# Kernel tuning notes

Hardware: AMD Instinct MI355X
Metric: run time of the kernel (lower is better)

The kernel has to match this reference:

```python
import jax, jax.numpy as jnp
import numpy as np

N_NODES = 50000
N_EDGES = 1600000
IN_DIM = 128
HID = 64   # per-head hidden/out dim
HEADS = 2
NEG_SLOPE = 0.2


def _gat_layer(x, src, dst, W, attn_l, attn_r, bias):
    # x: [N, Fin]; W: [Fin, H*D]; attn_l/attn_r: [H, D]; bias: [H, D]
    N = x.shape[0]
    H, D = attn_l.shape
    feat = (x @ W).reshape(N, H, D)                      # [N,H,D]
    el = jnp.sum(feat * attn_l, axis=-1)                 # [N,H]
    er = jnp.sum(feat * attn_r, axis=-1)                 # [N,H]
    e = jax.nn.leaky_relu(el[src] + er[dst], NEG_SLOPE)  # [E,H]
    # segment softmax over destination nodes
    m = jax.ops.segment_max(e, dst, num_segments=N)      # [N,H]
    ex = jnp.exp(e - m[dst])                             # [E,H]
    s = jax.ops.segment_sum(ex, dst, num_segments=N)     # [N,H]
    alpha = ex / s[dst]                                  # [E,H]
    msg = feat[src] * alpha[..., None]                   # [E,H,D]
    out = jax.ops.segment_sum(msg, dst, num_segments=N)  # [N,H,D]
    out = out + bias                                     # per-head bias
    # encoder: mean over heads, then ELU
    return jax.nn.elu(out.mean(axis=1))                  # [N,D]


def setup_inputs() -> dict:
    key = jax.random.key(0)
    ks = jax.random.split(key, 12)
    features = jax.random.normal(ks[0], (N_NODES, IN_DIM), dtype=jnp.float32)
    src = jax.random.randint(ks[1], (N_EDGES,), 0, N_NODES, dtype=jnp.int32)
    dst = jax.random.randint(ks[2], (N_EDGES,), 0, N_NODES, dtype=jnp.int32)
    sc1 = 1.0 / np.sqrt(IN_DIM)
    sc2 = 1.0 / np.sqrt(HID)
    W1 = jax.random.normal(ks[3], (IN_DIM, HEADS * HID), dtype=jnp.float32) * sc1
    al1 = jax.random.normal(ks[4], (HEADS, HID), dtype=jnp.float32) * sc2
    ar1 = jax.random.normal(ks[5], (HEADS, HID), dtype=jnp.float32) * sc2
    b1 = jnp.zeros((HEADS, HID), dtype=jnp.float32)
    W2 = jax.random.normal(ks[6], (HID, HEADS * HID), dtype=jnp.float32) * sc2
    al2 = jax.random.normal(ks[7], (HEADS, HID), dtype=jnp.float32) * sc2
    ar2 = jax.random.normal(ks[8], (HEADS, HID), dtype=jnp.float32) * sc2
    b2 = jnp.zeros((HEADS, HID), dtype=jnp.float32)
    return {"features": features, "W1": W1, "al1": al1, "ar1": ar1, "b1": b1,
            "W2": W2, "al2": al2, "ar2": ar2, "b2": b2, "src": src, "dst": dst}


def reference(features, W1, al1, ar1, b1, W2, al2, ar2, b2, src, dst):
    h = _gat_layer(features, src, dst, W1, al1, ar1, b1)  # [N, HID]
    h = _gat_layer(h, src, dst, W2, al2, ar2, b2)         # [N, HID]
    return h
```

## Files before the change

kernel.cpp:

```cpp
#include <hip/hip_runtime.h>
#include <hip/hip_fp16.h>
#include <math.h>

#define N_NODES 50000
#define N_EDGES 1600000
#define SLOTS 96
#define NODES_PER_GRP 6250

typedef int v4i __attribute__((ext_vector_type(4)));


__global__ void zero_kernel(int* p, int n) {
    int i = blockIdx.x * blockDim.x + threadIdx.x;
    if (i < n) p[i] = 0;
}

__global__ __launch_bounds__(256) void fill_part_kernel(
    const int* __restrict__ src, const int* __restrict__ dst,
    int* __restrict__ cursor, int* __restrict__ ssrc, int E) {
    const int g = blockIdx.x & 7;
    const int bg = blockIdx.x >> 3;
    const int nbg = gridDim.x >> 3;
    const int lo = g * NODES_PER_GRP;
    const int hi = lo + NODES_PER_GRP;
    const v4i* d4 = (const v4i*)dst;
    const v4i* s4 = (const v4i*)src;
    const int E4 = E >> 2;

    for (int i = bg * 256 + threadIdx.x; i < E4; i += nbg * 256) {
        v4i d = __builtin_nontemporal_load(d4 + i);
        v4i s = __builtin_nontemporal_load(s4 + i);
        if (d.x >= lo && d.x < hi) {
            int p = atomicAdd(&cursor[d.x], 1);
            if (p < SLOTS) ssrc[d.x * SLOTS + p] = s.x;
        }
        if (d.y >= lo && d.y < hi) {
            int p = atomicAdd(&cursor[d.y], 1);
            if (p < SLOTS) ssrc[d.y * SLOTS + p] = s.y;
        }
        if (d.z >= lo && d.z < hi) {
            int p = atomicAdd(&cursor[d.z], 1);
            if (p < SLOTS) ssrc[d.z * SLOTS + p] = s.z;
        }
        if (d.w >= lo && d.w < hi) {
            int p = atomicAdd(&cursor[d.w], 1);
            if (p < SLOTS) ssrc[d.w * SLOTS + p] = s.w;
        }
    }
}


template <int K>
__global__ __launch_bounds__(256) void gemm_elr_kernel(
    const float* __restrict__ x,
    const float* __restrict__ W,
    const float* __restrict__ al,
    const float* __restrict__ ar,
    __half* __restrict__ feat,
    float* __restrict__ el,
    float* __restrict__ er,
    int N) {
    constexpr int LDX = K + 4;
    __shared__ float xs[32 * LDX];
    const int tid = threadIdx.x;
    const int node0 = blockIdx.x * 32;

    for (int i = tid; i < 32 * K / 4; i += 256) {
        int r = i / (K / 4), c4 = i % (K / 4);
        float4 v = make_float4(0.f, 0.f, 0.f, 0.f);
        if (node0 + r < N) v = *(const float4*)&x[(size_t)(node0 + r) * K + c4 * 4];
        *(float4*)&xs[r * LDX + c4 * 4] = v;
    }
    __syncthreads();

    const int tx = tid & 31;
    const int ty = tid >> 5;
    const int col = tx * 4;

    float acc[4][4];
#pragma unroll
    for (int r = 0; r < 4; ++r)
#pragma unroll
        for (int c = 0; c < 4; ++c) acc[r][c] = 0.f;

    for (int kb = 0; kb < K / 4; ++kb) {
        float4 w0 = *(const float4*)&W[(kb * 4 + 0) * 128 + col];
        float4 w1 = *(const float4*)&W[(kb * 4 + 1) * 128 + col];
        float4 w2 = *(const float4*)&W[(kb * 4 + 2) * 128 + col];
        float4 w3 = *(const float4*)&W[(kb * 4 + 3) * 128 + col];
        float4 xv[4];
#pragma unroll
        for (int r = 0; r < 4; ++r)
            xv[r] = *(const float4*)&xs[(ty * 4 + r) * LDX + kb * 4];
#pragma unroll
        for (int r = 0; r < 4; ++r) {
            acc[r][0] += xv[r].x * w0.x + xv[r].y * w1.x + xv[r].z * w2.x + xv[r].w * w3.x;
            acc[r][1] += xv[r].x * w0.y + xv[r].y * w1.y + xv[r].z * w2.y + xv[r].w * w3.y;
            acc[r][2] += xv[r].x * w0.z + xv[r].y * w1.z + xv[r].z * w2.z + xv[r].w * w3.z;
            acc[r][3] += xv[r].x * w0.w + xv[r].y * w1.w + xv[r].z * w2.w + xv[r].w * w3.w;
        }
    }

    float4 alv = *(const float4*)&al[col];
    float4 arv = *(const float4*)&ar[col];
    float elp[4], erp[4];
#pragma unroll
    for (int r = 0; r < 4; ++r) {
        int n = node0 + ty * 4 + r;
        float4 f = make_float4(acc[r][0], acc[r][1], acc[r][2], acc[r][3]);
        if (n < N) {
            __half2 p0 = __floats2half2_rn(f.x, f.y);
            __half2 p1 = __floats2half2_rn(f.z, f.w);
            union { __half2 h2[2]; uint2 u; } pk;
            pk.h2[0] = p0; pk.h2[1] = p1;
            *(uint2*)&feat[(size_t)n * 128 + col] = pk.u;
        }
        elp[r] = f.x * alv.x + f.y * alv.y + f.z * alv.z + f.w * alv.w;
        erp[r] = f.x * arv.x + f.y * arv.y + f.z * arv.z + f.w * arv.w;
    }
#pragma unroll
    for (int m = 1; m <= 8; m <<= 1) {
#pragma unroll
        for (int r = 0; r < 4; ++r) {
            elp[r] += __shfl_xor(elp[r], m, 64);
            erp[r] += __shfl_xor(erp[r], m, 64);
        }
    }
    int h = tx >> 4;
    if ((tx & 15) == 0) {
#pragma unroll
        for (int r = 0; r < 4; ++r) {
            int n = node0 + ty * 4 + r;
            if (n < N) {
                el[n * 2 + h] = elp[r];
                er[n * 2 + h] = erp[r];
            }
        }
    }
}


__global__ __launch_bounds__(256) void aggregate_kernel(
    const __half* __restrict__ feat,
    const float* __restrict__ el,
    const float* __restrict__ er,
    const int* __restrict__ deg,
    const int* __restrict__ ssrc,
    const float* __restrict__ bias,
    float* __restrict__ hout,
    int N) {
    const int wave = threadIdx.x >> 6;
    const int lane = threadIdx.x & 63;
    const int n = blockIdx.x * 4 + wave;
    if (n >= N) return;

    const int q = lane >> 4;
    const int ql = lane & 15;
    const int h = ql >> 3;
    const float er_h = er[n * 2 + h];
    const int start = n * SLOTS;
    int d = deg[n];
    if (d > SLOTS) d = SLOTS;

    float acc[8];
#pragma unroll
    for (int j = 0; j < 8; ++j) acc[j] = 0.f;
    float ssum = 0.f;

#pragma unroll 2
    for (int base = 0; base < d; base += 4) {
        int idx = base + q;
        bool valid = idx < d;
        int s = ssrc[start + (valid ? idx : 0)];
        float e = el[s * 2 + h] + er_h;
        e = e > 0.f ? e : 0.2f * e;
        float x = valid ? __expf(e) : 0.f;
        float4 raw = *(const float4*)(feat + (size_t)s * 128 + ql * 8);
        const __half2* hp = (const __half2*)&raw;
        float2 f0 = __half22float2(hp[0]);
        float2 f1 = __half22float2(hp[1]);
        float2 f2 = __half22float2(hp[2]);
        float2 f3 = __half22float2(hp[3]);
        ssum += x;
        acc[0] += x * f0.x; acc[1] += x * f0.y;
        acc[2] += x * f1.x; acc[3] += x * f1.y;
        acc[4] += x * f2.x; acc[5] += x * f2.y;
        acc[6] += x * f3.x; acc[7] += x * f3.y;
    }

#pragma unroll
    for (int m = 16; m <= 32; m <<= 1) {
#pragma unroll
        for (int j = 0; j < 8; ++j) acc[j] += __shfl_xor(acc[j], m, 64);
        ssum += __shfl_xor(ssum, m, 64);
    }

    float inv = (d > 0) ? 1.0f / ssum : 0.0f;
    float4 b0 = *(const float4*)&bias[ql * 8];
    float4 b1 = *(const float4*)&bias[ql * 8 + 4];
    float v[8];
    v[0] = acc[0] * inv + b0.x; v[1] = acc[1] * inv + b0.y;
    v[2] = acc[2] * inv + b0.z; v[3] = acc[3] * inv + b0.w;
    v[4] = acc[4] * inv + b1.x; v[5] = acc[5] * inv + b1.y;
    v[6] = acc[6] * inv + b1.z; v[7] = acc[7] * inv + b1.w;

    float o[8];
#pragma unroll
    for (int j = 0; j < 8; ++j) {
        float p = __shfl_xor(v[j], 8, 64);
        float t = 0.5f * (v[j] + p);
        o[j] = t > 0.f ? t : expm1f(t);
    }
    if (lane < 8) {
        float4 w0 = make_float4(o[0], o[1], o[2], o[3]);
        float4 w1 = make_float4(o[4], o[5], o[6], o[7]);
        *(float4*)&hout[(size_t)n * 64 + ql * 8] = w0;
        *(float4*)&hout[(size_t)n * 64 + ql * 8 + 4] = w1;
    }
}


extern "C" void kernel_launch(void* const* d_in, const int* in_sizes, int n_in,
                              void* d_out, int out_size, void* d_ws, size_t ws_size,
                              hipStream_t stream) {
    const float* features = (const float*)d_in[0];
    const float* W1 = (const float*)d_in[1];
    const float* al1 = (const float*)d_in[2];
    const float* ar1 = (const float*)d_in[3];
    const float* b1 = (const float*)d_in[4];
    const float* W2 = (const float*)d_in[5];
    const float* al2 = (const float*)d_in[6];
    const float* ar2 = (const float*)d_in[7];
    const float* b2 = (const float*)d_in[8];
    const int* src = (const int*)d_in[9];
    const int* dst = (const int*)d_in[10];
    float* out = (float*)d_out;

    const int N = N_NODES;
    const int E = N_EDGES;

    char* ws = (char*)d_ws;
    size_t off = 0;
    auto alloc = [&](size_t bytes) {
        void* p = ws + off;
        off = (off + bytes + 255) & ~255ULL;
        return p;
    };
    int* cursor   = (int*)alloc((size_t)N * 4);
    int* ssrc     = (int*)alloc((size_t)N * SLOTS * 4);
    __half* feath = (__half*)alloc((size_t)N * 128 * 2);
    float* el     = (float*)alloc((size_t)N * 2 * 4);
    float* er     = (float*)alloc((size_t)N * 2 * 4);
    float* h1     = (float*)alloc((size_t)N * 64 * 4);

    zero_kernel<<<(N + 255) / 256, 256, 0, stream>>>(cursor, N);
    fill_part_kernel<<<2048, 256, 0, stream>>>(src, dst, cursor, ssrc, E);

    gemm_elr_kernel<128><<<(N + 31) / 32, 256, 0, stream>>>(features, W1, al1, ar1,
                                                            feath, el, er, N);
    aggregate_kernel<<<(N + 3) / 4, 256, 0, stream>>>(feath, el, er, cursor, ssrc,
                                                      b1, h1, N);
    gemm_elr_kernel<64><<<(N + 31) / 32, 256, 0, stream>>>(h1, W2, al2, ar2,
                                                           feath, el, er, N);
    aggregate_kernel<<<(N + 3) / 4, 256, 0, stream>>>(feath, el, er, cursor, ssrc,
                                                      b2, out, N);
}
```

Measured before the change: 412.0 us.

## Register-cache edge chunk and sweep destination sub-ranges in fill kernel

Each block now loads a contiguous chunk of src/dst edge vectors into registers once, then loops over 10 smaller destination-node sub-ranges. Inside each sub-range it issues the atomic cursor updates and slot writes, with a block barrier between sub-ranges. The goal is to tighten the working set of cursor/ssrc lines touched at a time and improve cache locality of scattered atomics. This adds more predicate checks per edge and extra barriers, and removes the nontemporal hints on the edge loads.

After: 547.8 us. +33.0%, slower.

```diff
diff --git a/kernel.cpp b/kernel.cpp
--- a/kernel.cpp
+++ b/kernel.cpp
@@ -6,6 +6,12 @@
 #define N_EDGES 1600000
 #define SLOTS 96
 #define NODES_PER_GRP 6250
+#define SUBS 10
+#define SUBW 625
+#define NBG 256
+#define E4T (N_EDGES / 4)
+#define CHUNK 1563
+#define PT 7
 
 typedef int v4i __attribute__((ext_vector_type(4)));
 
@@ -17,35 +23,53 @@
 
 __global__ __launch_bounds__(256) void fill_part_kernel(
     const int* __restrict__ src, const int* __restrict__ dst,
-    int* __restrict__ cursor, int* __restrict__ ssrc, int E) {
+    int* __restrict__ cursor, int* __restrict__ ssrc) {
     const int g = blockIdx.x & 7;
     const int bg = blockIdx.x >> 3;
-    const int nbg = gridDim.x >> 3;
-    const int lo = g * NODES_PER_GRP;
-    const int hi = lo + NODES_PER_GRP;
+    const int lo0 = g * NODES_PER_GRP;
     const v4i* d4 = (const v4i*)dst;
     const v4i* s4 = (const v4i*)src;
-    const int E4 = E >> 2;
-
-    for (int i = bg * 256 + threadIdx.x; i < E4; i += nbg * 256) {
-        v4i d = __builtin_nontemporal_load(d4 + i);
-        v4i s = __builtin_nontemporal_load(s4 + i);
-        if (d.x >= lo && d.x < hi) {
-            int p = atomicAdd(&cursor[d.x], 1);
-            if (p < SLOTS) ssrc[d.x * SLOTS + p] = s.x;
-        }
-        if (d.y >= lo && d.y < hi) {
-            int p = atomicAdd(&cursor[d.y], 1);
-            if (p < SLOTS) ssrc[d.y * SLOTS + p] = s.y;
-        }
-        if (d.z >= lo && d.z < hi) {
-            int p = atomicAdd(&cursor[d.z], 1);
-            if (p < SLOTS) ssrc[d.z * SLOTS + p] = s.z;
-        }
-        if (d.w >= lo && d.w < hi) {
-            int p = atomicAdd(&cursor[d.w], 1);
-            if (p < SLOTS) ssrc[d.w * SLOTS + p] = s.w;
-        }
+    const int base = bg * CHUNK;
+    const int elim = (base + CHUNK < E4T) ? base + CHUNK : E4T;
+
+    v4i dreg[PT], sreg[PT];
+#pragma unroll
+    for (int j = 0; j < PT; ++j) {
+        int i = base + j * 256 + (int)threadIdx.x;
+        if (i < elim) {
+            dreg[j] = d4[i];
+            sreg[j] = s4[i];
+        } else {
+            dreg[j] = (v4i){-1, -1, -1, -1};
+        }
+    }
+
+#pragma unroll 1
+    for (int sub = 0; sub < SUBS; ++sub) {
+        const int lo = lo0 + sub * SUBW;
+        const int hi = lo + SUBW;
+#pragma unroll
+        for (int j = 0; j < PT; ++j) {
+            v4i d = dreg[j];
+            v4i s = sreg[j];
+            if (d.x >= lo && d.x < hi) {
+                int p = atomicAdd(&cursor[d.x], 1);
+                if (p < SLOTS) ssrc[d.x * SLOTS + p] = s.x;
+            }
+            if (d.y >= lo && d.y < hi) {
+                int p = atomicAdd(&cursor[d.y], 1);
+                if (p < SLOTS) ssrc[d.y * SLOTS + p] = s.y;
+            }
+            if (d.z >= lo && d.z < hi) {
+                int p = atomicAdd(&cursor[d.z], 1);
+                if (p < SLOTS) ssrc[d.z * SLOTS + p] = s.z;
+            }
+            if (d.w >= lo && d.w < hi) {
+                int p = atomicAdd(&cursor[d.w], 1);
+                if (p < SLOTS) ssrc[d.w * SLOTS + p] = s.w;
+            }
+        }
+        __syncthreads();
     }
 }
 
@@ -237,7 +261,6 @@
     float* out = (float*)d_out;
 
     const int N = N_NODES;
-    const int E = N_EDGES;
 
     char* ws = (char*)d_ws;
     size_t off = 0;
@@ -254,7 +277,7 @@
     float* h1     = (float*)alloc((size_t)N * 64 * 4);
 
     zero_kernel<<<(N + 255) / 256, 256, 0, stream>>>(cursor, N);
-    fill_part_kernel<<<2048, 256, 0, stream>>>(src, dst, cursor, ssrc, E);
+    fill_part_kernel<<<NBG * 8, 256, 0, stream>>>(src, dst, cursor, ssrc);
 
     gemm_elr_kernel<128><<<(N + 31) / 32, 256, 0, stream>>>(features, W1, al1, ar1,
                                                             feath, el, er, N);
```

## Partition edge bucketing by hardware XCD with dynamic chunked work stealing

Applied to the files above, without the earlier changes.

The fill kernel used to map node groups to blocks via blockIdx modulo 8. It now reads the hardware XCC ID so each block starts on the node partition owned by its own XCD, which keeps cursor atomics and ssrc writes local to that XCD's L2. Blocks grab 2048-vec4 chunks from per-partition atomic work counters and move on to other partitions once their own is drained. In exchange there are extra __syncthreads and a global atomic per chunk, and the hardware register read depends on the architecture.

Result: slower. 581.6 us (+41.2%).

```diff
diff --git a/kernel.cpp b/kernel.cpp
--- a/kernel.cpp
+++ b/kernel.cpp
@@ -6,6 +6,8 @@
 #define N_EDGES 1600000
 #define SLOTS 96
 #define NODES_PER_GRP 6250
+#define E4T (N_EDGES / 4)
+#define CH4 2048
 
 typedef int v4i __attribute__((ext_vector_type(4)));
 
@@ -15,36 +17,56 @@
     if (i < n) p[i] = 0;
 }
 
-__global__ __launch_bounds__(256) void fill_part_kernel(
+__device__ __forceinline__ int get_xcd() {
+    int x;
+    asm volatile("s_getreg_b32 %0, hwreg(HW_REG_XCC_ID)" : "=s"(x));
+    return x & 7;
+}
+
+__global__ __launch_bounds__(256) void fill_xcd_kernel(
     const int* __restrict__ src, const int* __restrict__ dst,
-    int* __restrict__ cursor, int* __restrict__ ssrc, int E) {
-    const int g = blockIdx.x & 7;
-    const int bg = blockIdx.x >> 3;
-    const int nbg = gridDim.x >> 3;
-    const int lo = g * NODES_PER_GRP;
-    const int hi = lo + NODES_PER_GRP;
+    int* __restrict__ cursor, int* __restrict__ ssrc,
+    int* __restrict__ work) {
+    const int xcd = get_xcd();
     const v4i* d4 = (const v4i*)dst;
     const v4i* s4 = (const v4i*)src;
-    const int E4 = E >> 2;
-
-    for (int i = bg * 256 + threadIdx.x; i < E4; i += nbg * 256) {
-        v4i d = __builtin_nontemporal_load(d4 + i);
-        v4i s = __builtin_nontemporal_load(s4 + i);
-        if (d.x >= lo && d.x < hi) {
-            int p = atomicAdd(&cursor[d.x], 1);
-            if (p < SLOTS) ssrc[d.x * SLOTS + p] = s.x;
-        }
-        if (d.y >= lo && d.y < hi) {
-            int p = atomicAdd(&cursor[d.y], 1);
-            if (p < SLOTS) ssrc[d.y * SLOTS + p] = s.y;
-        }
-        if (d.z >= lo && d.z < hi) {
-            int p = atomicAdd(&cursor[d.z], 1);
-            if (p < SLOTS) ssrc[d.z * SLOTS + p] = s.z;
-        }
-        if (d.w >= lo && d.w < hi) {
-            int p = atomicAdd(&cursor[d.w], 1);
-            if (p < SLOTS) ssrc[d.w * SLOTS + p] = s.w;
+    __shared__ int sbase;
+
+    for (int qi = 0; qi < 8; ++qi) {
+        const int q = (xcd + qi) & 7;
+        const int lo = q * NODES_PER_GRP;
+        const int hi = lo + NODES_PER_GRP;
+        for (;;) {
+            if (threadIdx.x == 0) sbase = atomicAdd(&work[q], CH4);
+            __syncthreads();
+            const int base = sbase;
+            __syncthreads();
+            if (base >= E4T) break;
+            const int lim = (base + CH4 < E4T) ? base + CH4 : E4T;
+#pragma unroll
+            for (int k = 0; k < CH4 / 256; ++k) {
+                const int i = base + k * 256 + (int)threadIdx.x;
+                if (i < lim) {
+                    v4i d = __builtin_nontemporal_load(d4 + i);
+                    v4i s = __builtin_nontemporal_load(s4 + i);
+                    if (d.x >= lo && d.x < hi) {
+                        int p = atomicAdd(&cursor[d.x], 1);
+                        if (p < SLOTS) ssrc[d.x * SLOTS + p] = s.x;
+                    }
+                    if (d.y >= lo && d.y < hi) {
+                        int p = atomicAdd(&cursor[d.y], 1);
+                        if (p < SLOTS) ssrc[d.y * SLOTS + p] = s.y;
+                    }
+                    if (d.z >= lo && d.z < hi) {
+                        int p = atomicAdd(&cursor[d.z], 1);
+                        if (p < SLOTS) ssrc[d.z * SLOTS + p] = s.z;
+                    }
+                    if (d.w >= lo && d.w < hi) {
+                        int p = atomicAdd(&cursor[d.w], 1);
+                        if (p < SLOTS) ssrc[d.w * SLOTS + p] = s.w;
+                    }
+                }
+            }
         }
     }
 }
@@ -237,7 +259,6 @@
     float* out = (float*)d_out;
 
     const int N = N_NODES;
-    const int E = N_EDGES;
 
     char* ws = (char*)d_ws;
     size_t off = 0;
@@ -246,15 +267,16 @@
         off = (off + bytes + 255) & ~255ULL;
         return p;
     };
-    int* cursor   = (int*)alloc((size_t)N * 4);
+    int* cursor   = (int*)alloc((size_t)(N + 8) * 4);
+    int* work     = cursor + N;
     int* ssrc     = (int*)alloc((size_t)N * SLOTS * 4);
     __half* feath = (__half*)alloc((size_t)N * 128 * 2);
     float* el     = (float*)alloc((size_t)N * 2 * 4);
     float* er     = (float*)alloc((size_t)N * 2 * 4);
     float* h1     = (float*)alloc((size_t)N * 64 * 4);
 
-    zero_kernel<<<(N + 255) / 256, 256, 0, stream>>>(cursor, N);
-    fill_part_kernel<<<2048, 256, 0, stream>>>(src, dst, cursor, ssrc, E);
+    zero_kernel<<<(N + 8 + 255) / 256, 256, 0, stream>>>(cursor, N + 8);
+    fill_xcd_kernel<<<2048, 256, 0, stream>>>(src, dst, cursor, ssrc, work);
 
     gemm_elr_kernel<128><<<(N + 31) / 32, 256, 0, stream>>>(features, W1, al1, ar1,
                                                             feath, el, er, N);
```

## Process 8 edges per wave in aggregation and batch atomics in CSR fill

Applied to the files above, without the earlier changes.

The aggregate kernel now assigns 8 lanes per edge, each loading 32 bytes of fp16 features, so a wave handles 8 edges per iteration instead of 4. This halves loop trips and puts more gathers in flight, at the cost of twice as many accumulator registers and an extra shuffle-reduction stage. The fill kernel issues all four atomics before any of the dependent stores, so atomic latencies overlap. Its grid also shrinks from 2048 to 832 blocks.

Result: no change. 411.9 us (-0.0%).

```diff
diff --git a/kernel.cpp b/kernel.cpp
--- a/kernel.cpp
+++ b/kernel.cpp
@@ -30,22 +30,19 @@
     for (int i = bg * 256 + threadIdx.x; i < E4; i += nbg * 256) {
         v4i d = __builtin_nontemporal_load(d4 + i);
         v4i s = __builtin_nontemporal_load(s4 + i);
-        if (d.x >= lo && d.x < hi) {
-            int p = atomicAdd(&cursor[d.x], 1);
-            if (p < SLOTS) ssrc[d.x * SLOTS + p] = s.x;
-        }
-        if (d.y >= lo && d.y < hi) {
-            int p = atomicAdd(&cursor[d.y], 1);
-            if (p < SLOTS) ssrc[d.y * SLOTS + p] = s.y;
-        }
-        if (d.z >= lo && d.z < hi) {
-            int p = atomicAdd(&cursor[d.z], 1);
-            if (p < SLOTS) ssrc[d.z * SLOTS + p] = s.z;
-        }
-        if (d.w >= lo && d.w < hi) {
-            int p = atomicAdd(&cursor[d.w], 1);
-            if (p < SLOTS) ssrc[d.w * SLOTS + p] = s.w;
-        }
+        const bool c0 = d.x >= lo && d.x < hi;
+        const bool c1 = d.y >= lo && d.y < hi;
+        const bool c2 = d.z >= lo && d.z < hi;
+        const bool c3 = d.w >= lo && d.w < hi;
+        int p0, p1, p2, p3;
+        if (c0) p0 = atomicAdd(&cursor[d.x], 1);
+        if (c1) p1 = atomicAdd(&cursor[d.y], 1);
+        if (c2) p2 = atomicAdd(&cursor[d.z], 1);
+        if (c3) p3 = atomicAdd(&cursor[d.w], 1);
+        if (c0 && p0 < SLOTS) ssrc[d.x * SLOTS + p0] = s.x;
+        if (c1 && p1 < SLOTS) ssrc[d.y * SLOTS + p1] = s.y;
+        if (c2 && p2 < SLOTS) ssrc[d.z * SLOTS + p2] = s.z;
+        if (c3 && p3 < SLOTS) ssrc[d.w * SLOTS + p3] = s.w;
     }
 }
 
@@ -154,68 +151,74 @@
     const int n = blockIdx.x * 4 + wave;
     if (n >= N) return;
 
-    const int q = lane >> 4;
-    const int ql = lane & 15;
-    const int h = ql >> 3;
+    const int q = lane >> 3;
+    const int ql = lane & 7;
+    const int h = ql >> 2;
     const float er_h = er[n * 2 + h];
     const int start = n * SLOTS;
     int d = deg[n];
     if (d > SLOTS) d = SLOTS;
 
-    float acc[8];
-#pragma unroll
-    for (int j = 0; j < 8; ++j) acc[j] = 0.f;
+    float acc[16];
+#pragma unroll
+    for (int j = 0; j < 16; ++j) acc[j] = 0.f;
     float ssum = 0.f;
 
-#pragma unroll 2
-    for (int base = 0; base < d; base += 4) {
+    for (int base = 0; base < d; base += 8) {
         int idx = base + q;
         bool valid = idx < d;
         int s = ssrc[start + (valid ? idx : 0)];
         float e = el[s * 2 + h] + er_h;
         e = e > 0.f ? e : 0.2f * e;
         float x = valid ? __expf(e) : 0.f;
-        float4 raw = *(const float4*)(feat + (size_t)s * 128 + ql * 8);
-        const __half2* hp = (const __half2*)&raw;
-        float2 f0 = __half22float2(hp[0]);
-        float2 f1 = __half22float2(hp[1]);
-        float2 f2 = __half22float2(hp[2]);
-        float2 f3 = __half22float2(hp[3]);
+        const float4* fp = (const float4*)(feat + (size_t)s * 128 + ql * 16);
+        float4 ra = fp[0];
+        float4 rb = fp[1];
+        const __half2* ha = (const __half2*)&ra;
+        const __half2* hb = (const __half2*)&rb;
         ssum += x;
-        acc[0] += x * f0.x; acc[1] += x * f0.y;
-        acc[2] += x * f1.x; acc[3] += x * f1.y;
-        acc[4] += x * f2.x; acc[5] += x * f2.y;
-        acc[6] += x * f3.x; acc[7] += x * f3.y;
-    }
-
-#pragma unroll
-    for (int m = 16; m <= 32; m <<= 1) {
-#pragma unroll
-        for (int j = 0; j < 8; ++j) acc[j] += __shfl_xor(acc[j], m, 64);
+#pragma unroll
+        for (int j = 0; j < 4; ++j) {
+            float2 fa = __half22float2(ha[j]);
+            float2 fb = __half22float2(hb[j]);
+            acc[j * 2 + 0] += x * fa.x;
+            acc[j * 2 + 1] += x * fa.y;
+            acc[8 + j * 2 + 0] += x * fb.x;
+            acc[8 + j * 2 + 1] += x * fb.y;
+        }
+    }
+
+#pragma unroll
+    for (int m = 8; m <= 32; m <<= 1) {
+#pragma unroll
+        for (int j = 0; j < 16; ++j) acc[j] += __shfl_xor(acc[j], m, 64);
         ssum += __shfl_xor(ssum, m, 64);
     }
 
     float inv = (d > 0) ? 1.0f / ssum : 0.0f;
-    float4 b0 = *(const float4*)&bias[ql * 8];
-    float4 b1 = *(const float4*)&bias[ql * 8 + 4];
-    float v[8];
-    v[0] = acc[0] * inv + b0.x; v[1] = acc[1] * inv + b0.y;
-    v[2] = acc[2] * inv + b0.z; v[3] = acc[3] * inv + b0.w;
-    v[4] = acc[4] * inv + b1.x; v[5] = acc[5] * inv + b1.y;
-    v[6] = acc[6] * inv + b1.z; v[7] = acc[7] * inv + b1.w;
-
-    float o[8];
-#pragma unroll
-    for (int j = 0; j < 8; ++j) {
-        float p = __shfl_xor(v[j], 8, 64);
+    float v[16];
+#pragma unroll
+    for (int j = 0; j < 4; ++j) {
+        float4 b = *(const float4*)&bias[ql * 16 + j * 4];
+        v[j * 4 + 0] = acc[j * 4 + 0] * inv + b.x;
+        v[j * 4 + 1] = acc[j * 4 + 1] * inv + b.y;
+        v[j * 4 + 2] = acc[j * 4 + 2] * inv + b.z;
+        v[j * 4 + 3] = acc[j * 4 + 3] * inv + b.w;
+    }
+
+    float o[16];
+#pragma unroll
+    for (int j = 0; j < 16; ++j) {
+        float p = __shfl_xor(v[j], 4, 64);
         float t = 0.5f * (v[j] + p);
         o[j] = t > 0.f ? t : expm1f(t);
     }
-    if (lane < 8) {
-        float4 w0 = make_float4(o[0], o[1], o[2], o[3]);
-        float4 w1 = make_float4(o[4], o[5], o[6], o[7]);
-        *(float4*)&hout[(size_t)n * 64 + ql * 8] = w0;
-        *(float4*)&hout[(size_t)n * 64 + ql * 8 + 4] = w1;
+    if (lane < 4) {
+#pragma unroll
+        for (int j = 0; j < 4; ++j) {
+            float4 w = make_float4(o[j * 4 + 0], o[j * 4 + 1], o[j * 4 + 2], o[j * 4 + 3]);
+            *(float4*)&hout[(size_t)n * 64 + ql * 16 + j * 4] = w;
+        }
     }
 }
 
@@ -254,7 +257,7 @@
     float* h1     = (float*)alloc((size_t)N * 64 * 4);
 
     zero_kernel<<<(N + 255) / 256, 256, 0, stream>>>(cursor, N);
-    fill_part_kernel<<<2048, 256, 0, stream>>>(src, dst, cursor, ssrc, E);
+    fill_part_kernel<<<8 * 104, 256, 0, stream>>>(src, dst, cursor, ssrc, E);
 
     gemm_elr_kernel<128><<<(N + 31) / 32, 256, 0, stream>>>(features, W1, al1, ar1,
                                                             feath, el, er, N);
```
